# Kernel tuning notes

Hardware: AMD Instinct MI355X
Metric: run time of the kernel (lower is better)

Reference implementation:

```python
import jax, jax.numpy as jnp
import numpy as np

H = 256          # hidden_dim
D = 64           # dim_dynamic
R = 49           # pooler_resolution ** 2
N = 2000         # bs * num_proposals
EPS = 1e-5


def _ln(x, g, b):
    m = jnp.mean(x, axis=-1, keepdims=True)
    v = jnp.mean(jnp.square(x - m), axis=-1, keepdims=True)
    return (x - m) * jax.lax.rsqrt(v + EPS) * g + b


def setup_inputs() -> dict:
    key = jax.random.key(0)
    ks = jax.random.split(key, 6)
    pro_features = jax.random.normal(ks[0], (1, N, H), dtype=jnp.float32)
    roi_features = jax.random.normal(ks[1], (R, N, H), dtype=jnp.float32)
    # dynamic_layer: Linear(H, num_dynamic * H * D) with num_dynamic = 2
    W_dyn = jax.random.normal(ks[2], (H, 2 * H * D), dtype=jnp.float32) * 0.02
    b_dyn = jnp.zeros((2 * H * D,), dtype=jnp.float32)
    # out_layer: Linear(H * R, H)
    W_out = jax.random.normal(ks[3], (H * R, H), dtype=jnp.float32) * 0.02
    b_out = jnp.zeros((H,), dtype=jnp.float32)
    g1 = jnp.ones((D,), dtype=jnp.float32); b1 = jnp.zeros((D,), dtype=jnp.float32)
    g2 = jnp.ones((H,), dtype=jnp.float32); b2 = jnp.zeros((H,), dtype=jnp.float32)
    g3 = jnp.ones((H,), dtype=jnp.float32); b3 = jnp.zeros((H,), dtype=jnp.float32)
    return {"pro_features": pro_features, "roi_features": roi_features,
            "W_dyn": W_dyn, "b_dyn": b_dyn, "W_out": W_out, "b_out": b_out,
            "g1": g1, "b1": b1, "g2": g2, "b2": b2, "g3": g3, "b3": b3}


def reference(pro_features, roi_features, W_dyn, b_dyn, W_out, b_out,
              g1, b1, g2, b2, g3, b3):
    # roi_features: (R, N, H) -> features: (N, R, H)
    feats = jnp.transpose(roi_features, (1, 0, 2))
    # per-instance dynamic parameters: (N, 2*H*D)
    params = pro_features[0] @ W_dyn + b_dyn
    num_params = H * D
    p1 = params[:, :num_params].reshape(-1, H, D)   # (N, H, D)
    p2 = params[:, num_params:].reshape(-1, D, H)   # (N, D, H)
    f = jnp.einsum('nrh,nhd->nrd', feats, p1)       # bmm 1
    f = jax.nn.relu(_ln(f, g1, b1))
    f = jnp.einsum('nrd,ndh->nrh', f, p2)           # bmm 2
    f = jax.nn.relu(_ln(f, g2, b2))
    f = f.reshape(f.shape[0], R * H)                # flatten(1)
    f = jax.nn.relu(_ln(f @ W_out + b_out, g3, b3))
    return f  # (N, H)
```

## Files before the change

### kernel.cpp

```cpp
#include <hip/hip_runtime.h>

typedef unsigned short u16;
typedef __attribute__((ext_vector_type(8))) short short8;
typedef __attribute__((ext_vector_type(4))) float f32x4;

#define N_INST 2000
#define H_DIM 256
#define D_DIM 64
#define R_DIM 49
#define LN_EPS 1e-5f
#define SPLITK 14

__device__ __forceinline__ u16 f2bf(float f) {
  union { float f; unsigned int i; } x; x.f = f;
  unsigned int r = x.i + 0x7fffu + ((x.i >> 16) & 1u);
  return (u16)(r >> 16);
}
__device__ __forceinline__ float bf2f(u16 u) {
  union { unsigned int i; float f; } x; x.i = ((unsigned int)u) << 16; return x.f;
}
__device__ __forceinline__ short8 ld8(const u16* p) {
  return *reinterpret_cast<const short8*>(p);
}
__device__ __forceinline__ short8 pack8(float4 a, float4 b) {
  short8 r;
  r[0] = (short)f2bf(a.x); r[1] = (short)f2bf(a.y);
  r[2] = (short)f2bf(a.z); r[3] = (short)f2bf(a.w);
  r[4] = (short)f2bf(b.x); r[5] = (short)f2bf(b.y);
  r[6] = (short)f2bf(b.z); r[7] = (short)f2bf(b.w);
  return r;
}
__device__ __forceinline__ f32x4 mfma16(short8 a, short8 b, f32x4 c) {
  return __builtin_amdgcn_mfma_f32_16x16x32_bf16(a, b, c, 0, 0, 0);
}
__device__ __forceinline__ void wave_reduce2(float& s, float& s2) {
#pragma unroll
  for (int off = 32; off > 0; off >>= 1) {
    s  += __shfl_down(s, off);
    s2 += __shfl_down(s2, off);
  }
  s = __shfl(s, 0); s2 = __shfl(s2, 0);
}
__device__ __forceinline__ void gload16(const u16* g, u16* l) {
  __builtin_amdgcn_global_load_lds(
      (const __attribute__((address_space(1))) void*)g,
      (__attribute__((address_space(3))) void*)l, 16, 0, 0);
}

__global__ __launch_bounds__(256) void cast_pro(const float* __restrict__ in,
                                                u16* __restrict__ out, int n4) {
  for (int i = blockIdx.x * 256 + threadIdx.x; i < n4; i += gridDim.x * 256) {
    float4 v = ((const float4*)in)[i];
    u16* op = out + i * 4;
    op[0] = f2bf(v.x); op[1] = f2bf(v.y); op[2] = f2bf(v.z); op[3] = f2bf(v.w);
  }
}

__global__ __launch_bounds__(256) void cast_wdyn(const float* __restrict__ W,
                                                 u16* __restrict__ WT, int half) {
  __shared__ u16 T[64][65];
  const int tid = threadIdx.x;
  const int wave = tid >> 6, lane = tid & 63;
  const int b = blockIdx.x;
  const int kt = b >> 8;
  long colbase, rowbase; int rstride;
  if (half == 0) {
    int h = b & 255;
    colbase = (long)h * 64; rowbase = h; rstride = 256;
  } else {
    int d = b & 63, hc = (b >> 6) & 3;
    colbase = 16384L + d * 256 + hc * 64;
    rowbase = 16384L + hc * 4096 + d; rstride = 64;
  }
#pragma unroll
  for (int i = 0; i < 16; ++i) {
    int kk = wave * 16 + i;
    int k = kt * 64 + kk;
    T[kk][lane] = f2bf(W[(long)k * 32768 + colbase + lane]);
  }
  __syncthreads();
#pragma unroll
  for (int i = 0; i < 16; ++i) {
    int jj = wave * 16 + i;
    long ro = rowbase + (long)jj * rstride;
    WT[ro * 256 + kt * 64 + lane] = T[lane][jj];
  }
}

__global__ __launch_bounds__(256) void cast_wout(const float* __restrict__ W,
                                                 u16* __restrict__ WT) {
  __shared__ u16 T[64][65];
  const int tid = threadIdx.x;
  const int wave = tid >> 6, lane = tid & 63;
  const int kt = blockIdx.x >> 2, ct = blockIdx.x & 3;
#pragma unroll
  for (int i = 0; i < 16; ++i) {
    int kk = wave * 16 + i;
    long k = (long)kt * 64 + kk;
    T[kk][lane] = f2bf(W[k * 256 + ct * 64 + lane]);
  }
  __syncthreads();
#pragma unroll
  for (int i = 0; i < 16; ++i) {
    int cc = wave * 16 + i;
    long c = (long)ct * 64 + cc;
    WT[c * 12544 + (long)kt * 64 + lane] = T[lane][cc];
  }
}

__global__ __launch_bounds__(256, 3) void gemm128(
    const u16* __restrict__ A, int lda, int M,
    const u16* __restrict__ BT, int ldbt,
    const float* __restrict__ bias, int bias_mode,
    void* __restrict__ Cout, int ldc, long c_stride_s,
    int ksteps, int n_blocks, int out_f32)
{
  union Smem {
    struct { u16 a[2][128 * 32]; u16 b[2][128 * 32]; } s;
    u16 cb[128 * 128];
  };
  __shared__ Smem sm;

  const int tid = threadIdx.x;
  const int wave = tid >> 6, lane = tid & 63;
  const int quad = lane >> 4, l16 = lane & 15;
  const int wm = wave >> 1, wn = wave & 1;
  const int bid = blockIdx.x;
  const int mblk = bid / n_blocks, nblk = bid - mblk * n_blocks;
  const int m0 = mblk * 128, n0 = nblk * 128;
  const int s = blockIdx.y;
  const int kb = s * ksteps * 32;

  const int cl = tid & 3;
  const int r0 = tid >> 2, r1 = 64 + (tid >> 2);
  const int cg0 = cl ^ ((r0 >> 1) & 3);
  const int cg1 = cl ^ ((r1 >> 1) & 3);
  int ga0 = m0 + r0; if (ga0 >= M) ga0 = M - 1;
  int ga1 = m0 + r1; if (ga1 >= M) ga1 = M - 1;
  const u16* gA0 = A + (long)ga0 * lda + kb + cg0 * 8;
  const u16* gA1 = A + (long)ga1 * lda + kb + cg1 * 8;
  const u16* gB0 = BT + (long)(n0 + r0) * ldbt + kb + cg0 * 8;
  const u16* gB1 = BT + (long)(n0 + r1) * ldbt + kb + cg1 * 8;

  int fAoff[4], fBoff[4];
#pragma unroll
  for (int i = 0; i < 4; ++i) {
    int rt = wm * 64 + i * 16 + l16;
    fAoff[i] = rt * 32 + (quad ^ ((rt >> 1) & 3)) * 8;
    int ct = wn * 64 + i * 16 + l16;
    fBoff[i] = ct * 32 + (quad ^ ((ct >> 1) & 3)) * 8;
  }

  f32x4 acc[4][4];
#pragma unroll
  for (int mi = 0; mi < 4; ++mi)
#pragma unroll
    for (int ni = 0; ni < 4; ++ni) acc[mi][ni] = f32x4{0.f, 0.f, 0.f, 0.f};

  gload16(gA0, &sm.s.a[0][tid * 8]);
  gload16(gA1, &sm.s.a[0][(tid + 256) * 8]);
  gload16(gB0, &sm.s.b[0][tid * 8]);
  gload16(gB1, &sm.s.b[0][(tid + 256) * 8]);

  for (int ks = 0; ks < ksteps; ++ks) {
    const int cur = ks & 1, nxt = cur ^ 1;
    __syncthreads();
    if (ks + 1 < ksteps) {
      const int ko = (ks + 1) * 32;
      gload16(gA0 + ko, &sm.s.a[nxt][tid * 8]);
      gload16(gA1 + ko, &sm.s.a[nxt][(tid + 256) * 8]);
      gload16(gB0 + ko, &sm.s.b[nxt][tid * 8]);
      gload16(gB1 + ko, &sm.s.b[nxt][(tid + 256) * 8]);
    }
    short8 av[4], bv[4];
#pragma unroll
    for (int i = 0; i < 4; ++i) {
      av[i] = ld8(&sm.s.a[cur][fAoff[i]]);
      bv[i] = ld8(&sm.s.b[cur][fBoff[i]]);
    }
#pragma unroll
    for (int mi = 0; mi < 4; ++mi)
#pragma unroll
      for (int ni = 0; ni < 4; ++ni)
        acc[mi][ni] = mfma16(av[mi], bv[ni], acc[mi][ni]);
  }

  if (!out_f32) {
    float bvv[4];
#pragma unroll
    for (int ni = 0; ni < 4; ++ni) {
      int col = n0 + wn * 64 + ni * 16 + l16;
      int bi = col;
      if (bias_mode == 1)      bi = ((col & 255) << 6) + (col >> 8);
      else if (bias_mode == 2) bi = 16384 + ((col & 63) << 8) + (col >> 6);
      bvv[ni] = bias ? bias[bi] : 0.f;
    }
    __syncthreads();
#pragma unroll
    for (int mi = 0; mi < 4; ++mi)
#pragma unroll
      for (int ni = 0; ni < 4; ++ni)
#pragma unroll
        for (int i = 0; i < 4; ++i) {
          int row = wm * 64 + mi * 16 + quad * 4 + i;
          int col = wn * 64 + ni * 16 + l16;
          sm.cb[row * 128 + col] = f2bf(acc[mi][ni][i] + bvv[ni]);
        }
    __syncthreads();
    u16* Cp = (u16*)Cout;
#pragma unroll
    for (int j = 0; j < 8; ++j) {
      int lin = j * 2048 + tid * 8;
      int row = lin >> 7, col = lin & 127;
      int grow = m0 + row;
      if (grow < M)
        *reinterpret_cast<short8*>(Cp + (long)grow * ldc + n0 + col) =
            ld8(&sm.cb[lin]);
    }
  } else {
    float* Cp = (float*)Cout + (long)s * c_stride_s;
#pragma unroll
    for (int mi = 0; mi < 4; ++mi)
#pragma unroll
      for (int ni = 0; ni < 4; ++ni) {
        int col = n0 + wn * 64 + ni * 16 + l16;
#pragma unroll
        for (int i = 0; i < 4; ++i) {
          int row = m0 + wm * 64 + mi * 16 + quad * 4 + i;
          if (row < M) Cp[(long)row * ldc + col] = acc[mi][ni][i];
        }
      }
  }
}

__global__ __launch_bounds__(256) void bmm1_ln(
    const float* __restrict__ roi,
    const u16* __restrict__ P1T,
    const float* __restrict__ g1, const float* __restrict__ b1,
    u16* __restrict__ f1n)
{
  const int n = blockIdx.x;
  const int tid = threadIdx.x;
  const int wave = tid >> 6, lane = tid & 63;
  const int quad = lane >> 4, l16 = lane & 15;

  union SmemU {
    u16 bt[D_DIM * H_DIM];
    float cb[64][D_DIM];
  };
  __shared__ SmemU sm;

  int r = wave * 16 + l16;
  int rr = (r < R_DIM) ? r : 0;
  const float* Arow = roi + ((long)rr * N_INST + n) * H_DIM + quad * 8;
  float4 rv[16];
#pragma unroll
  for (int ks = 0; ks < 8; ++ks) {
    rv[2 * ks]     = ((const float4*)(Arow + ks * 32))[0];
    rv[2 * ks + 1] = ((const float4*)(Arow + ks * 32))[1];
  }

  const u16* P1n = P1T + (long)n * (H_DIM * D_DIM);
#pragma unroll
  for (int j = 0; j < 8; ++j) {
    int lc = j * 256 + tid;
    int d = lc >> 5, c = lc & 31;
    int cg = (c & 24) | ((c & 7) ^ (d & 7));
    gload16(P1n + d * 256 + cg * 8, &sm.bt[lc * 8]);
  }
  __syncthreads();

  f32x4 acc[4];
#pragma unroll
  for (int i = 0; i < 4; ++i) acc[i] = f32x4{0.f, 0.f, 0.f, 0.f};

#pragma unroll
  for (int ks = 0; ks < 8; ++ks) {
    short8 af = pack8(rv[2 * ks], rv[2 * ks + 1]);
#pragma unroll
    for (int sub = 0; sub < 4; ++sub) {
      int d = sub * 16 + l16;
      int q = ks * 4 + quad;
      int c = (q & 24) | ((q & 7) ^ (d & 7));
      short8 bf = ld8(&sm.bt[d * 256 + c * 8]);
      acc[sub] = mfma16(af, bf, acc[sub]);
    }
  }
  __syncthreads();
#pragma unroll
  for (int sub = 0; sub < 4; ++sub)
#pragma unroll
    for (int i = 0; i < 4; ++i)
      sm.cb[wave * 16 + quad * 4 + i][sub * 16 + l16] = acc[sub][i];
  __syncthreads();

  float gv = g1[lane], bv = b1[lane];
  for (int i = 0; i < 13; ++i) {
    int r2 = wave + 4 * i;
    if (r2 < R_DIM) {
      float x = sm.cb[r2][lane];
      float sv = x, s2 = x * x;
      wave_reduce2(sv, s2);
      float mean = sv * (1.f / 64.f);
      float var = s2 * (1.f / 64.f) - mean * mean;
      float rs = rsqrtf(var + LN_EPS);
      float y = fmaxf((x - mean) * rs * gv + bv, 0.f);
      f1n[((long)n * R_DIM + r2) * D_DIM + lane] = f2bf(y);
    }
  }
}

__global__ __launch_bounds__(256) void bmm2_ln(
    const u16* __restrict__ f1n,
    const u16* __restrict__ P2T,
    const float* __restrict__ g2, const float* __restrict__ b2,
    u16* __restrict__ f2n)
{
  const int n = blockIdx.x;
  const int tid = threadIdx.x;
  const int wave = tid >> 6, lane = tid & 63;
  const int quad = lane >> 4, l16 = lane & 15;

  union SmemU {
    u16 bt[H_DIM * D_DIM];
    u16 cb[R_DIM][H_DIM];
  };
  __shared__ SmemU sm;

  int r = wave * 16 + l16;
  int rr = (r < R_DIM) ? r : 0;
  const u16* Arow = f1n + ((long)n * R_DIM + rr) * D_DIM + quad * 8;
  short8 af0 = ld8(Arow);
  short8 af1 = ld8(Arow + 32);

  const u16* P2n = P2T + (long)n * (D_DIM * H_DIM);
#pragma unroll
  for (int j = 0; j < 8; ++j) {
    int lc = j * 256 + tid;
    int h = lc >> 3, c = lc & 7;
    int cg = c ^ (h & 7);
    gload16(P2n + h * 64 + cg * 8, &sm.bt[lc * 8]);
  }
  __syncthreads();

  f32x4 acc[16];
#pragma unroll
  for (int i = 0; i < 16; ++i) acc[i] = f32x4{0.f, 0.f, 0.f, 0.f};

#pragma unroll
  for (int ks = 0; ks < 2; ++ks) {
    short8 af = ks ? af1 : af0;
#pragma unroll
    for (int sub = 0; sub < 16; ++sub) {
      int h = sub * 16 + l16;
      int c = (ks * 4 + quad) ^ (h & 7);
      short8 bf = ld8(&sm.bt[h * 64 + c * 8]);
      acc[sub] = mfma16(af, bf, acc[sub]);
    }
  }
  __syncthreads();
#pragma unroll
  for (int sub = 0; sub < 16; ++sub)
#pragma unroll
    for (int i = 0; i < 4; ++i) {
      int row = wave * 16 + quad * 4 + i;
      if (row < R_DIM) sm.cb[row][sub * 16 + l16] = f2bf(acc[sub][i]);
    }
  __syncthreads();

  float4 gv = *(const float4*)&g2[lane * 4];
  float4 bv = *(const float4*)&b2[lane * 4];
  for (int i = 0; i < 13; ++i) {
    int r2 = wave + 4 * i;
    if (r2 < R_DIM) {
      ushort4 xv = *reinterpret_cast<const ushort4*>(&sm.cb[r2][lane * 4]);
      float x0 = bf2f(xv.x), x1 = bf2f(xv.y), x2 = bf2f(xv.z), x3 = bf2f(xv.w);
      float sv = x0 + x1 + x2 + x3;
      float s2 = x0 * x0 + x1 * x1 + x2 * x2 + x3 * x3;
      wave_reduce2(sv, s2);
      float mean = sv * (1.f / 256.f);
      float var = s2 * (1.f / 256.f) - mean * mean;
      float rs = rsqrtf(var + LN_EPS);
      ushort4 yv;
      yv.x = f2bf(fmaxf((x0 - mean) * rs * gv.x + bv.x, 0.f));
      yv.y = f2bf(fmaxf((x1 - mean) * rs * gv.y + bv.y, 0.f));
      yv.z = f2bf(fmaxf((x2 - mean) * rs * gv.z + bv.z, 0.f));
      yv.w = f2bf(fmaxf((x3 - mean) * rs * gv.w + bv.w, 0.f));
      *reinterpret_cast<ushort4*>(
          &f2n[((long)n * R_DIM + r2) * H_DIM + lane * 4]) = yv;
    }
  }
}

__global__ __launch_bounds__(64) void ln3_k(
    const float* __restrict__ partial,
    const float* __restrict__ b_out,
    const float* __restrict__ g3, const float* __restrict__ b3,
    float* __restrict__ out)
{
  const int n = blockIdx.x;
  const int lane = threadIdx.x;
  float x[4], sv = 0.f, s2 = 0.f;
#pragma unroll
  for (int j = 0; j < 4; ++j) {
    int h = lane + 64 * j;
    float v = b_out[h];
#pragma unroll
    for (int ss = 0; ss < SPLITK; ++ss)
      v += partial[((long)ss * N_INST + n) * H_DIM + h];
    x[j] = v; sv += v; s2 += v * v;
  }
  wave_reduce2(sv, s2);
  float mean = sv * (1.f / 256.f);
  float var = s2 * (1.f / 256.f) - mean * mean;
  float rs = rsqrtf(var + LN_EPS);
#pragma unroll
  for (int j = 0; j < 4; ++j) {
    int h = lane + 64 * j;
    float y = fmaxf((x[j] - mean) * rs * g3[h] + b3[h], 0.f);
    out[(long)n * H_DIM + h] = y;
  }
}

extern "C" void kernel_launch(void* const* d_in, const int* in_sizes, int n_in,
                              void* d_out, int out_size, void* d_ws, size_t ws_size,
                              hipStream_t stream) {
  const float* pro  = (const float*)d_in[0];
  const float* roi  = (const float*)d_in[1];
  const float* Wdyn = (const float*)d_in[2];
  const float* bdyn = (const float*)d_in[3];
  const float* Wout = (const float*)d_in[4];
  const float* bout = (const float*)d_in[5];
  const float* g1 = (const float*)d_in[6];
  const float* b1 = (const float*)d_in[7];
  const float* g2 = (const float*)d_in[8];
  const float* b2 = (const float*)d_in[9];
  const float* g3 = (const float*)d_in[10];
  const float* b3 = (const float*)d_in[11];
  float* out = (float*)d_out;

  char* ws = (char*)d_ws;
  u16* proB   = (u16*)ws;
  u16* WdynT  = (u16*)(ws + 1024000);
  u16* WoutT  = (u16*)(ws + 17801216);
  u16* params = (u16*)(ws + 24223744);
  u16* f1n    = (u16*)(ws + 89759744);
  u16* f2n    = (u16*)(ws + 102303744);
  float* partial = (float*)(ws + 24223744);

  dim3 blk(256);
  const int HD = H_DIM * D_DIM;

  cast_pro<<<dim3(500), blk, 0, stream>>>(pro, proB, 512000 / 4);
  cast_wdyn<<<dim3(1024), blk, 0, stream>>>(Wdyn, WdynT, 0);
  cast_wdyn<<<dim3(1024), blk, 0, stream>>>(Wdyn, WdynT, 1);
  cast_wout<<<dim3(784), blk, 0, stream>>>(Wout, WoutT);

  gemm128<<<dim3(16 * 128, 1), blk, 0, stream>>>(
      proB, H_DIM, N_INST, WdynT, H_DIM, bdyn, 1,
      (void*)params, HD, 0L, 8, 128, 0);
  bmm1_ln<<<dim3(N_INST), blk, 0, stream>>>(roi, params, g1, b1, f1n);
  gemm128<<<dim3(16 * 128, 1), blk, 0, stream>>>(
      proB, H_DIM, N_INST, WdynT + (long)16384 * 256, H_DIM, bdyn, 2,
      (void*)params, HD, 0L, 8, 128, 0);
  bmm2_ln<<<dim3(N_INST), blk, 0, stream>>>(f1n, params, g2, b2, f2n);
  gemm128<<<dim3(16 * 2, SPLITK), blk, 0, stream>>>(
      f2n, R_DIM * H_DIM, N_INST, WoutT, R_DIM * H_DIM, nullptr, 0,
      (void*)partial, H_DIM, (long)N_INST * H_DIM, 28, 2, 1);
  ln3_k<<<dim3(N_INST), dim3(64), 0, stream>>>(partial, bout, g3, b3, out);
}
```

Before: 345.6 us.

## Fuse both dynamic bmm+LN stages into one kernel and merge param GEMMs

Merges the two dynamic-parameter GEMMs into a single launch that writes P1 and P2 for each instance into one contiguous 32768-element buffer, using a new bias mode. Fuses bmm1+LN1 and bmm2+LN2 into one kernel, so the f1 intermediate stays in shared memory and never goes to global memory. The LN statistics are computed straight from MFMA accumulators with 16-lane shuffles, and the P2 load is issued early so it overlaps LN1. The cost is a larger params buffer (about 131 MB), which must be written and read back in one pass and so has worse cache locality than the old per-half reuse, plus a launch-bounds occupancy hint.

```diff
diff --git a/kernel.cpp b/kernel.cpp
--- a/kernel.cpp
+++ b/kernel.cpp
@@ -191,8 +191,9 @@
     for (int ni = 0; ni < 4; ++ni) {
       int col = n0 + wn * 64 + ni * 16 + l16;
       int bi = col;
-      if (bias_mode == 1)      bi = ((col & 255) << 6) + (col >> 8);
-      else if (bias_mode == 2) bi = 16384 + ((col & 63) << 8) + (col >> 6);
+      if (bias_mode == 3)
+        bi = (col < 16384) ? (((col & 255) << 6) + (col >> 8))
+                           : (16384 + ((col & 63) << 8) + ((col >> 6) & 255));
       bvv[ni] = bias ? bias[bi] : 0.f;
     }
     __syncthreads();
@@ -233,162 +234,181 @@
   }
 }
 
-__global__ __launch_bounds__(256) void bmm1_ln(
+__global__ __launch_bounds__(256, 3) void bmm12_ln(
     const float* __restrict__ roi,
-    const u16* __restrict__ P1T,
+    const u16* __restrict__ P12,
     const float* __restrict__ g1, const float* __restrict__ b1,
-    u16* __restrict__ f1n)
+    const float* __restrict__ g2, const float* __restrict__ b2,
+    u16* __restrict__ f2n)
 {
+  __shared__ u16 reg0[16384];
+  __shared__ u16 f1buf[4096];
   const int n = blockIdx.x;
   const int tid = threadIdx.x;
   const int wave = tid >> 6, lane = tid & 63;
   const int quad = lane >> 4, l16 = lane & 15;
-
-  union SmemU {
-    u16 bt[D_DIM * H_DIM];
-    float cb[64][D_DIM];
-  };
-  __shared__ SmemU sm;
-
-  int r = wave * 16 + l16;
-  int rr = (r < R_DIM) ? r : 0;
-  const float* Arow = roi + ((long)rr * N_INST + n) * H_DIM + quad * 8;
-  float4 rv[16];
-#pragma unroll
-  for (int ks = 0; ks < 8; ++ks) {
-    rv[2 * ks]     = ((const float4*)(Arow + ks * 32))[0];
-    rv[2 * ks + 1] = ((const float4*)(Arow + ks * 32))[1];
-  }
-
-  const u16* P1n = P1T + (long)n * (H_DIM * D_DIM);
+  const int wstripe = wave * 16;
+
+  const u16* P1n = P12 + (long)n * 32768;
 #pragma unroll
   for (int j = 0; j < 8; ++j) {
     int lc = j * 256 + tid;
     int d = lc >> 5, c = lc & 31;
     int cg = (c & 24) | ((c & 7) ^ (d & 7));
-    gload16(P1n + d * 256 + cg * 8, &sm.bt[lc * 8]);
-  }
-  __syncthreads();
-
-  f32x4 acc[4];
-#pragma unroll
-  for (int i = 0; i < 4; ++i) acc[i] = f32x4{0.f, 0.f, 0.f, 0.f};
-
+    gload16(P1n + d * 256 + cg * 8, &reg0[lc * 8]);
+  }
+  int r = wstripe + l16;
+  int rr = (r < R_DIM) ? r : 0;
+  const float* Arow = roi + ((long)rr * N_INST + n) * H_DIM + quad * 8;
+  float4 rv[16];
 #pragma unroll
   for (int ks = 0; ks < 8; ++ks) {
-    short8 af = pack8(rv[2 * ks], rv[2 * ks + 1]);
+    rv[2 * ks]     = ((const float4*)(Arow + ks * 32))[0];
+    rv[2 * ks + 1] = ((const float4*)(Arow + ks * 32))[1];
+  }
+  float gv1[4], bv1[4];
+#pragma unroll
+  for (int sub = 0; sub < 4; ++sub) {
+    gv1[sub] = g1[sub * 16 + l16]; bv1[sub] = b1[sub * 16 + l16];
+  }
+  __syncthreads();
+
+  short8 sa[8];
+#pragma unroll
+  for (int ks = 0; ks < 8; ++ks) sa[ks] = pack8(rv[2 * ks], rv[2 * ks + 1]);
+
+  f32x4 acc1[4];
+#pragma unroll
+  for (int i = 0; i < 4; ++i) acc1[i] = f32x4{0.f, 0.f, 0.f, 0.f};
+#pragma unroll
+  for (int ks = 0; ks < 8; ++ks) {
 #pragma unroll
     for (int sub = 0; sub < 4; ++sub) {
       int d = sub * 16 + l16;
       int q = ks * 4 + quad;
       int c = (q & 24) | ((q & 7) ^ (d & 7));
-      short8 bf = ld8(&sm.bt[d * 256 + c * 8]);
-      acc[sub] = mfma16(af, bf, acc[sub]);
-    }
-  }
-  __syncthreads();
-#pragma unroll
-  for (int sub = 0; sub < 4; ++sub)
-#pragma unroll
-    for (int i = 0; i < 4; ++i)
-      sm.cb[wave * 16 + quad * 4 + i][sub * 16 + l16] = acc[sub][i];
-  __syncthreads();
-
-  float gv = g1[lane], bv = b1[lane];
-  for (int i = 0; i < 13; ++i) {
-    int r2 = wave + 4 * i;
-    if (r2 < R_DIM) {
-      float x = sm.cb[r2][lane];
-      float sv = x, s2 = x * x;
-      wave_reduce2(sv, s2);
-      float mean = sv * (1.f / 64.f);
-      float var = s2 * (1.f / 64.f) - mean * mean;
-      float rs = rsqrtf(var + LN_EPS);
-      float y = fmaxf((x - mean) * rs * gv + bv, 0.f);
-      f1n[((long)n * R_DIM + r2) * D_DIM + lane] = f2bf(y);
-    }
-  }
-}
-
-__global__ __launch_bounds__(256) void bmm2_ln(
-    const u16* __restrict__ f1n,
-    const u16* __restrict__ P2T,
-    const float* __restrict__ g2, const float* __restrict__ b2,
-    u16* __restrict__ f2n)
-{
-  const int n = blockIdx.x;
-  const int tid = threadIdx.x;
-  const int wave = tid >> 6, lane = tid & 63;
-  const int quad = lane >> 4, l16 = lane & 15;
-
-  union SmemU {
-    u16 bt[H_DIM * D_DIM];
-    u16 cb[R_DIM][H_DIM];
-  };
-  __shared__ SmemU sm;
-
-  int r = wave * 16 + l16;
-  int rr = (r < R_DIM) ? r : 0;
-  const u16* Arow = f1n + ((long)n * R_DIM + rr) * D_DIM + quad * 8;
-  short8 af0 = ld8(Arow);
-  short8 af1 = ld8(Arow + 32);
-
-  const u16* P2n = P2T + (long)n * (D_DIM * H_DIM);
+      acc1[sub] = mfma16(sa[ks], ld8(&reg0[d * 256 + c * 8]), acc1[sub]);
+    }
+  }
+  __syncthreads();
+
+  const u16* P2n = P12 + (long)n * 32768 + 16384;
 #pragma unroll
   for (int j = 0; j < 8; ++j) {
     int lc = j * 256 + tid;
     int h = lc >> 3, c = lc & 7;
-    int cg = c ^ (h & 7);
-    gload16(P2n + h * 64 + cg * 8, &sm.bt[lc * 8]);
-  }
-  __syncthreads();
-
-  f32x4 acc[16];
-#pragma unroll
-  for (int i = 0; i < 16; ++i) acc[i] = f32x4{0.f, 0.f, 0.f, 0.f};
-
+    gload16(P2n + h * 64 + (c ^ (h & 7)) * 8, &reg0[lc * 8]);
+  }
+
+  {
+    float s1[4], s2[4];
+#pragma unroll
+    for (int i = 0; i < 4; ++i) {
+      s1[i] = 0.f; s2[i] = 0.f;
+#pragma unroll
+      for (int sub = 0; sub < 4; ++sub) {
+        float v = acc1[sub][i]; s1[i] += v; s2[i] += v * v;
+      }
+    }
+#pragma unroll
+    for (int m = 1; m < 16; m <<= 1)
+#pragma unroll
+      for (int i = 0; i < 4; ++i) {
+        s1[i] += __shfl_xor(s1[i], m, 16);
+        s2[i] += __shfl_xor(s2[i], m, 16);
+      }
+#pragma unroll
+    for (int i = 0; i < 4; ++i) {
+      float mean = s1[i] * (1.f / 64.f);
+      float var = s2[i] * (1.f / 64.f) - mean * mean;
+      float rs = rsqrtf(var + LN_EPS);
+      int row = wstripe + quad * 4 + i;
+#pragma unroll
+      for (int sub = 0; sub < 4; ++sub) {
+        float y = fmaxf((acc1[sub][i] - mean) * rs * gv1[sub] + bv1[sub], 0.f);
+        int kc = (sub * 2 + (l16 >> 3)) ^ (row & 7);
+        f1buf[row * 64 + kc * 8 + (l16 & 7)] = f2bf(y);
+      }
+    }
+  }
+  __syncthreads();
+
+  short8 af2[2];
 #pragma unroll
   for (int ks = 0; ks < 2; ++ks) {
-    short8 af = ks ? af1 : af0;
+    int row = wstripe + l16;
+    int c2 = (ks * 4 + quad) ^ (row & 7);
+    af2[ks] = ld8(&f1buf[row * 64 + c2 * 8]);
+  }
+  f32x4 acc2[16];
+#pragma unroll
+  for (int i = 0; i < 16; ++i) acc2[i] = f32x4{0.f, 0.f, 0.f, 0.f};
+#pragma unroll
+  for (int ks = 0; ks < 2; ++ks) {
 #pragma unroll
     for (int sub = 0; sub < 16; ++sub) {
       int h = sub * 16 + l16;
       int c = (ks * 4 + quad) ^ (h & 7);
-      short8 bf = ld8(&sm.bt[h * 64 + c * 8]);
-      acc[sub] = mfma16(af, bf, acc[sub]);
-    }
-  }
-  __syncthreads();
-#pragma unroll
-  for (int sub = 0; sub < 16; ++sub)
+      acc2[sub] = mfma16(af2[ks], ld8(&reg0[h * 64 + c * 8]), acc2[sub]);
+    }
+  }
+
+  float mean2[4], rs2[4];
+  {
+    float s1[4], s2[4];
 #pragma unroll
     for (int i = 0; i < 4; ++i) {
-      int row = wave * 16 + quad * 4 + i;
-      if (row < R_DIM) sm.cb[row][sub * 16 + l16] = f2bf(acc[sub][i]);
-    }
-  __syncthreads();
-
-  float4 gv = *(const float4*)&g2[lane * 4];
-  float4 bv = *(const float4*)&b2[lane * 4];
-  for (int i = 0; i < 13; ++i) {
-    int r2 = wave + 4 * i;
-    if (r2 < R_DIM) {
-      ushort4 xv = *reinterpret_cast<const ushort4*>(&sm.cb[r2][lane * 4]);
-      float x0 = bf2f(xv.x), x1 = bf2f(xv.y), x2 = bf2f(xv.z), x3 = bf2f(xv.w);
-      float sv = x0 + x1 + x2 + x3;
-      float s2 = x0 * x0 + x1 * x1 + x2 * x2 + x3 * x3;
-      wave_reduce2(sv, s2);
-      float mean = sv * (1.f / 256.f);
-      float var = s2 * (1.f / 256.f) - mean * mean;
-      float rs = rsqrtf(var + LN_EPS);
-      ushort4 yv;
-      yv.x = f2bf(fmaxf((x0 - mean) * rs * gv.x + bv.x, 0.f));
-      yv.y = f2bf(fmaxf((x1 - mean) * rs * gv.y + bv.y, 0.f));
-      yv.z = f2bf(fmaxf((x2 - mean) * rs * gv.z + bv.z, 0.f));
-      yv.w = f2bf(fmaxf((x3 - mean) * rs * gv.w + bv.w, 0.f));
-      *reinterpret_cast<ushort4*>(
-          &f2n[((long)n * R_DIM + r2) * H_DIM + lane * 4]) = yv;
-    }
+      s1[i] = 0.f; s2[i] = 0.f;
+#pragma unroll
+      for (int sub = 0; sub < 16; ++sub) {
+        float v = acc2[sub][i]; s1[i] += v; s2[i] += v * v;
+      }
+    }
+#pragma unroll
+    for (int m = 1; m < 16; m <<= 1)
+#pragma unroll
+      for (int i = 0; i < 4; ++i) {
+        s1[i] += __shfl_xor(s1[i], m, 16);
+        s2[i] += __shfl_xor(s2[i], m, 16);
+      }
+#pragma unroll
+    for (int i = 0; i < 4; ++i) {
+      mean2[i] = s1[i] * (1.f / 256.f);
+      float var = s2[i] * (1.f / 256.f) - mean2[i] * mean2[i];
+      rs2[i] = rsqrtf(var + LN_EPS);
+    }
+  }
+  __syncthreads();
+
+#pragma unroll
+  for (int i = 0; i < 4; ++i) {
+    int row = wstripe + quad * 4 + i;
+    if (row < R_DIM) {
+#pragma unroll
+      for (int sub = 0; sub < 16; ++sub)
+        reg0[row * 264 + sub * 16 + l16] =
+            f2bf((acc2[sub][i] - mean2[i]) * rs2[i]);
+    }
+  }
+  __syncthreads();
+
+  u16* f2out = f2n + (long)n * (R_DIM * H_DIM);
+  for (int t = tid; t < R_DIM * 32; t += 256) {
+    int row = t >> 5, c = t & 31;
+    short8 z8 = ld8(&reg0[row * 264 + c * 8]);
+    const float4* gp = (const float4*)(g2 + c * 8);
+    const float4* bp = (const float4*)(b2 + c * 8);
+    float4 ga = gp[0], gb = gp[1], ba = bp[0], bb = bp[1];
+    short8 y;
+    y[0] = (short)f2bf(fmaxf(bf2f((u16)z8[0]) * ga.x + ba.x, 0.f));
+    y[1] = (short)f2bf(fmaxf(bf2f((u16)z8[1]) * ga.y + ba.y, 0.f));
+    y[2] = (short)f2bf(fmaxf(bf2f((u16)z8[2]) * ga.z + ba.z, 0.f));
+    y[3] = (short)f2bf(fmaxf(bf2f((u16)z8[3]) * ga.w + ba.w, 0.f));
+    y[4] = (short)f2bf(fmaxf(bf2f((u16)z8[4]) * gb.x + bb.x, 0.f));
+    y[5] = (short)f2bf(fmaxf(bf2f((u16)z8[5]) * gb.y + bb.y, 0.f));
+    y[6] = (short)f2bf(fmaxf(bf2f((u16)z8[6]) * gb.z + bb.z, 0.f));
+    y[7] = (short)f2bf(fmaxf(bf2f((u16)z8[7]) * gb.w + bb.w, 0.f));
+    *reinterpret_cast<short8*>(f2out + row * 256 + c * 8) = y;
   }
 }
 
@@ -440,30 +460,24 @@
   float* out = (float*)d_out;
 
   char* ws = (char*)d_ws;
-  u16* proB   = (u16*)ws;
-  u16* WdynT  = (u16*)(ws + 1024000);
-  u16* WoutT  = (u16*)(ws + 17801216);
-  u16* params = (u16*)(ws + 24223744);
-  u16* f1n    = (u16*)(ws + 89759744);
-  u16* f2n    = (u16*)(ws + 102303744);
+  u16* proB  = (u16*)ws;
+  u16* WdynT = (u16*)(ws + 1024000);
+  u16* WoutT = (u16*)(ws + 17801216);
+  u16* P12   = (u16*)(ws + 24223744);
+  u16* f2n   = (u16*)(ws + 155295744);
   float* partial = (float*)(ws + 24223744);
 
   dim3 blk(256);
-  const int HD = H_DIM * D_DIM;
 
   cast_pro<<<dim3(500), blk, 0, stream>>>(pro, proB, 512000 / 4);
   cast_wdyn<<<dim3(1024), blk, 0, stream>>>(Wdyn, WdynT, 0);
   cast_wdyn<<<dim3(1024), blk, 0, stream>>>(Wdyn, WdynT, 1);
   cast_wout<<<dim3(784), blk, 0, stream>>>(Wout, WoutT);
 
-  gemm128<<<dim3(16 * 128, 1), blk, 0, stream>>>(
-      proB, H_DIM, N_INST, WdynT, H_DIM, bdyn, 1,
-      (void*)params, HD, 0L, 8, 128, 0);
-  bmm1_ln<<<dim3(N_INST), blk, 0, stream>>>(roi, params, g1, b1, f1n);
-  gemm128<<<dim3(16 * 128, 1), blk, 0, stream>>>(
-      proB, H_DIM, N_INST, WdynT + (long)16384 * 256, H_DIM, bdyn, 2,
-      (void*)params, HD, 0L, 8, 128, 0);
-  bmm2_ln<<<dim3(N_INST), blk, 0, stream>>>(f1n, params, g2, b2, f2n);
+  gemm128<<<dim3(16 * 256, 1), blk, 0, stream>>>(
+      proB, H_DIM, N_INST, WdynT, H_DIM, bdyn, 3,
+      (void*)P12, 32768, 0L, 8, 256, 0);
+  bmm12_ln<<<dim3(N_INST), blk, 0, stream>>>(roi, P12, g1, b1, g2, b2, f2n);
   gemm128<<<dim3(16 * 2, SPLITK), blk, 0, stream>>>(
       f2n, R_DIM * H_DIM, N_INST, WoutT, R_DIM * H_DIM, nullptr, 0,
       (void*)partial, H_DIM, (long)N_INST * H_DIM, 28, 2, 1);
```

Result: faster. 337.1 us (-2.5%).
